# Kernel optimization log

Measured on AMD Instinct MI355X. Metric: run time of the kernel, lower is better.

## Reference

```python
import jax, jax.numpy as jnp
import numpy as np

B, S, D, H = 4, 2048, 1024, 16
HD = D // H

def setup_inputs() -> dict:
    key = jax.random.key(0)
    ks = jax.random.split(key, 11)
    s = 1.0 / np.sqrt(D)
    def lin(k):
        kw, kb = jax.random.split(k)
        return (jax.random.uniform(kw, (D, D), jnp.float32, -s, s),
                jax.random.uniform(kb, (D,), jnp.float32, -s, s))
    Wq, bq = lin(ks[0]); Wk, bk = lin(ks[1]); Wv, bv = lin(ks[2]); Wo, bo = lin(ks[3])
    return {
        "query": jax.random.normal(ks[4], (B, S, D), jnp.float32),
        "key": jax.random.normal(ks[5], (B, S, D), jnp.float32),
        "value": jax.random.normal(ks[6], (B, S, D), jnp.float32),
        "Wq": Wq, "bq": bq, "Wk": Wk, "bk": bk,
        "Wv": Wv, "bv": bv, "Wo": Wo, "bo": bo,
    }

def reference(query, key, value, Wq, bq, Wk, bk, Wv, bv, Wo, bo):
    def split_heads(x):  # [B,S,D] -> [B,H,S,HD]
        return x.reshape(B, S, H, HD).transpose(0, 2, 1, 3)
    q = split_heads(query @ Wq + bq)
    k = split_heads(key @ Wk + bk)
    v = split_heads(value @ Wv + bv)
    scores = jnp.einsum('bhqd,bhkd->bhqk', q, k) / np.sqrt(HD)
    probs = jax.nn.softmax(scores, axis=-1)
    ctx = jnp.einsum('bhqk,bhkd->bhqd', probs, v)
    ctx = ctx.transpose(0, 2, 1, 3).reshape(B, S, D)
    return ctx @ Wo + bo
```

## Files before the change

kernel.cpp:

```cpp
#include <hip/hip_runtime.h>
#include <hip/hip_bf16.h>

#define B_ 4
#define S_ 2048
#define D_ 1024
#define H_ 16
#define HD_ 64
#define M_ (B_*S_)

typedef __bf16 bf16;
typedef bf16 bf16x8 __attribute__((ext_vector_type(8)));
typedef bf16 bf16x4 __attribute__((ext_vector_type(4)));
typedef float f32x4 __attribute__((ext_vector_type(4)));

__device__ __forceinline__ void gload_lds16(const void* g, void* l) {
  __builtin_amdgcn_global_load_lds((const __attribute__((address_space(1))) void*)g,
                                   (__attribute__((address_space(3))) void*)l, 16, 0, 0);
}

__global__ __launch_bounds__(256)
void wtrans_kernel(const float* __restrict__ Wq, const float* __restrict__ Wk,
                   const float* __restrict__ Wv, const float* __restrict__ Wo,
                   bf16* __restrict__ Wqt, bf16* __restrict__ Wkt,
                   bf16* __restrict__ Wvt, bf16* __restrict__ Wot) {
  __shared__ float tile[64][68];
  const float* W; bf16* Wt;
  switch (blockIdx.z) {
    case 0: W = Wq; Wt = Wqt; break;
    case 1: W = Wk; Wt = Wkt; break;
    case 2: W = Wv; Wt = Wvt; break;
    default: W = Wo; Wt = Wot; break;
  }
  const int n0 = blockIdx.x * 64, k0 = blockIdx.y * 64;
  const int tid = threadIdx.x;
#pragma unroll
  for (int i = 0; i < 4; i++) {
    int f = tid + i * 256;
    int k = f >> 4, c = f & 15;
    float4 v = *(const float4*)(W + (size_t)(k0 + k) * D_ + n0 + c * 4);
    *(float4*)(&tile[k][c * 4]) = v;
  }
  __syncthreads();
#pragma unroll
  for (int i = 0; i < 2; i++) {
    int f = tid + i * 256;
    int n = f >> 3, c = f & 7;
    bf16x8 o;
#pragma unroll
    for (int j = 0; j < 8; j++) o[j] = (bf16)tile[c * 8 + j][n];
    *(bf16x8*)(Wt + (size_t)(n0 + n) * D_ + k0 + c * 8) = o;
  }
}

#define QSCALE 0.18033688011112042f

__global__ __launch_bounds__(256)
void proj_gemm_kernel(const float* __restrict__ Aq, const float* __restrict__ Ak,
                      const float* __restrict__ Av,
                      const bf16* __restrict__ Wqt, const bf16* __restrict__ Wkt,
                      const bf16* __restrict__ Wvt,
                      const float* __restrict__ bq, const float* __restrict__ bk,
                      const float* __restrict__ bv,
                      bf16* __restrict__ qb, bf16* __restrict__ kb, bf16* __restrict__ vbT) {
  __shared__ bf16 As[128 * 64];
  __shared__ bf16 Bs[128 * 64];
  const float* A; const bf16* Bt; const float* bias;
  if (blockIdx.z == 0)      { A = Aq; Bt = Wqt; bias = bq; }
  else if (blockIdx.z == 1) { A = Ak; Bt = Wkt; bias = bk; }
  else                      { A = Av; Bt = Wvt; bias = bv; }

  const int n0 = blockIdx.x * 128, m0 = blockIdx.y * 128;
  const int tid = threadIdx.x;
  const int lane = tid & 63, w = tid >> 6;
  const int wr = w >> 1, wc = w & 1;
  const int l15 = lane & 15, quad = lane >> 4;
  const int srow = lane >> 3, schunk = lane & 7;

  f32x4 acc[4][4] = {};
  float4 Ar[4][2];

  auto loadA = [&](int kt) {
    const int k0 = kt * 64;
#pragma unroll
    for (int t = 0; t < 4; t++) {
      const float* p = A + (size_t)(m0 + w * 32 + t * 8 + srow) * D_ + k0 + schunk * 8;
      Ar[t][0] = *(const float4*)p;
      Ar[t][1] = *(const float4*)(p + 4);
    }
  };

  loadA(0);

  for (int kt = 0; kt < D_ / 64; kt++) {
    const int k0 = kt * 64;
#pragma unroll
    for (int t = 0; t < 4; t++) {
      int r0 = w * 32 + t * 8;
      int row = r0 + srow;
      int cg = schunk ^ (row & 7);
      gload_lds16(Bt + (size_t)(n0 + row) * D_ + k0 + cg * 8, &Bs[r0 * 64]);
    }
#pragma unroll
    for (int t = 0; t < 4; t++) {
      int row = w * 32 + t * 8 + srow;
      int c = schunk ^ (row & 7);
      bf16x8 v;
      v[0] = (bf16)Ar[t][0].x; v[1] = (bf16)Ar[t][0].y;
      v[2] = (bf16)Ar[t][0].z; v[3] = (bf16)Ar[t][0].w;
      v[4] = (bf16)Ar[t][1].x; v[5] = (bf16)Ar[t][1].y;
      v[6] = (bf16)Ar[t][1].z; v[7] = (bf16)Ar[t][1].w;
      *(bf16x8*)(&As[row * 64 + c * 8]) = v;
    }
    __syncthreads();

    if (kt + 1 < D_ / 64) loadA(kt + 1);

#pragma unroll
    for (int ks = 0; ks < 2; ks++) {
      bf16x8 a[4], b[4];
#pragma unroll
      for (int fm = 0; fm < 4; fm++) {
        int row = wr * 64 + fm * 16 + l15;
        a[fm] = *(const bf16x8*)(&As[row * 64 + (((ks * 4 + quad) ^ (row & 7)) * 8)]);
      }
#pragma unroll
      for (int fn = 0; fn < 4; fn++) {
        int row = wc * 64 + fn * 16 + l15;
        b[fn] = *(const bf16x8*)(&Bs[row * 64 + (((ks * 4 + quad) ^ (row & 7)) * 8)]);
      }
#pragma unroll
      for (int fm = 0; fm < 4; fm++)
#pragma unroll
        for (int fn = 0; fn < 4; fn++)
          acc[fm][fn] = __builtin_amdgcn_mfma_f32_16x16x32_bf16(a[fm], b[fn], acc[fm][fn], 0, 0, 0);
    }
    __syncthreads();
  }

  if (blockIdx.z < 2) {
    bf16* C = (blockIdx.z == 0) ? qb : kb;
    float scale = (blockIdx.z == 0) ? QSCALE : 1.0f;
#pragma unroll
    for (int fm = 0; fm < 4; fm++) {
      int row = m0 + wr * 64 + fm * 16 + quad * 4;
#pragma unroll
      for (int fn = 0; fn < 4; fn++) {
        int col = n0 + wc * 64 + fn * 16 + l15;
        float bval = bias[col];
#pragma unroll
        for (int r = 0; r < 4; r++)
          C[(size_t)(row + r) * D_ + col] = (bf16)((acc[fm][fn][r] + bval) * scale);
      }
    }
  } else {
#pragma unroll
    for (int fm = 0; fm < 4; fm++) {
      int row = m0 + wr * 64 + fm * 16 + quad * 4;
#pragma unroll
      for (int fn = 0; fn < 4; fn++) {
        int col = n0 + wc * 64 + fn * 16 + l15;
        float bval = bias[col];
        bf16x4 pk;
#pragma unroll
        for (int r = 0; r < 4; r++) pk[r] = (bf16)(acc[fm][fn][r] + bval);
        *(bf16x4*)(vbT + (size_t)col * M_ + row) = pk;
      }
    }
  }
}

__global__ __launch_bounds__(256)
void attn_kernel(const bf16* __restrict__ qb, const bf16* __restrict__ kb,
                 const bf16* __restrict__ vbT, bf16* __restrict__ ctxb) {
  __shared__ bf16 Ks[2][64 * 64];
  __shared__ bf16 Vs[2][64 * 64];
  __shared__ bf16 Ps[256 * 64];

  const int bh = blockIdx.y;
  const int b = bh >> 4, h = bh & 15;
  const int q0 = blockIdx.x * 256;
  const int tid = threadIdx.x, lane = tid & 63, w = tid >> 6;
  const int l15 = lane & 15, quad = lane >> 4;

  const size_t baseQ = ((size_t)(b * S_ + q0)) * D_ + h * HD_;

  bf16x8 qf[4][2];
#pragma unroll
  for (int fq = 0; fq < 4; fq++)
#pragma unroll
    for (int ks = 0; ks < 2; ks++)
      qf[fq][ks] = *(const bf16x8*)(qb + baseQ + (size_t)(w * 64 + fq * 16 + l15) * D_ + ks * 32 + quad * 8);

  f32x4 o[4][4] = {};
  float li[4] = {};

  const int srow_i = lane >> 3;
  const int schunk = lane & 7;

  auto stage = [&](int buf, int kt) {
#pragma unroll
    for (int t = 0; t < 2; t++) {
      const int r0 = w * 16 + t * 8;
      const int row = r0 + srow_i;
      const int c = schunk ^ (row & 7);
      const bf16* gK = kb + ((size_t)(b * S_ + kt * 64 + row)) * D_ + h * 64 + c * 8;
      gload_lds16(gK, &Ks[buf][r0 * 64]);
      const bf16* gV = vbT + ((size_t)(h * 64 + row)) * M_ + b * S_ + kt * 64 + c * 8;
      gload_lds16(gV, &Vs[buf][r0 * 64]);
    }
  };

  stage(0, 0);
  __syncthreads();

  for (int kt = 0; kt < S_ / 64; kt++) {
    const int buf = kt & 1;
    if (kt + 1 < S_ / 64) stage(buf ^ 1, kt + 1);

    f32x4 st[4][4] = {};
#pragma unroll
    for (int ks = 0; ks < 2; ks++) {
#pragma unroll
      for (int fk = 0; fk < 4; fk++) {
        const int key = fk * 16 + l15;
        bf16x8 kf = *(const bf16x8*)(&Ks[buf][key * 64 + (((ks * 4 + quad) ^ (key & 7)) * 8)]);
#pragma unroll
        for (int fq = 0; fq < 4; fq++)
          st[fk][fq] = __builtin_amdgcn_mfma_f32_16x16x32_bf16(kf, qf[fq][ks], st[fk][fq], 0, 0, 0);
      }
    }

#pragma unroll
    for (int fq = 0; fq < 4; fq++) {
      const int row = w * 64 + fq * 16 + l15;
#pragma unroll
      for (int fk = 0; fk < 4; fk++) {
        float p0 = __builtin_amdgcn_exp2f(st[fk][fq][0]);
        float p1 = __builtin_amdgcn_exp2f(st[fk][fq][1]);
        float p2 = __builtin_amdgcn_exp2f(st[fk][fq][2]);
        float p3 = __builtin_amdgcn_exp2f(st[fk][fq][3]);
        li[fq] += (p0 + p1) + (p2 + p3);
        bf16x4 pk;
        pk[0] = (bf16)p0; pk[1] = (bf16)p1; pk[2] = (bf16)p2; pk[3] = (bf16)p3;
        const int chunk = (fk * 2 + (quad >> 1)) ^ (row & 7);
        *(bf16x4*)(&Ps[row * 64 + chunk * 8 + (quad & 1) * 4]) = pk;
      }
    }

#pragma unroll
    for (int ks2 = 0; ks2 < 2; ks2++) {
      bf16x8 pf[4], vf[4];
#pragma unroll
      for (int fm = 0; fm < 4; fm++) {
        const int row = w * 64 + fm * 16 + l15;
        pf[fm] = *(const bf16x8*)(&Ps[row * 64 + (((ks2 * 4 + quad) ^ (row & 7)) * 8)]);
      }
#pragma unroll
      for (int fd = 0; fd < 4; fd++) {
        const int d = fd * 16 + l15;
        vf[fd] = *(const bf16x8*)(&Vs[buf][d * 64 + (((ks2 * 4 + quad) ^ (d & 7)) * 8)]);
      }
#pragma unroll
      for (int fm = 0; fm < 4; fm++)
#pragma unroll
        for (int fd = 0; fd < 4; fd++)
          o[fm][fd] = __builtin_amdgcn_mfma_f32_16x16x32_bf16(pf[fm], vf[fd], o[fm][fd], 0, 0, 0);
    }
    __syncthreads();
  }

  float linv[4];
#pragma unroll
  for (int fq = 0; fq < 4; fq++) {
    float l = li[fq];
    l += __shfl_xor(l, 16);
    l += __shfl_xor(l, 32);
    linv[fq] = 1.0f / l;
  }
#pragma unroll
  for (int fq = 0; fq < 4; fq++) {
#pragma unroll
    for (int r = 0; r < 4; r++) {
      float inv = __shfl(linv[fq], quad * 4 + r);
      int row = w * 64 + fq * 16 + quad * 4 + r;
#pragma unroll
      for (int fd = 0; fd < 4; fd++)
        ctxb[baseQ + (size_t)row * D_ + fd * 16 + l15] = (bf16)(o[fq][fd][r] * inv);
    }
  }
}

__global__ __launch_bounds__(256)
void out_gemm_kernel(const bf16* __restrict__ A, const bf16* __restrict__ Bt,
                     const float* __restrict__ bias, float* __restrict__ Cout) {
  __shared__ bf16 As[128 * 64];
  __shared__ bf16 Bs[128 * 64];
  const int n0 = blockIdx.x * 128, m0 = blockIdx.y * 128;
  const int tid = threadIdx.x;
  const int lane = tid & 63, w = tid >> 6;
  const int wr = w >> 1, wc = w & 1;
  const int l15 = lane & 15, quad = lane >> 4;
  const int srow = lane >> 3, schunk = lane & 7;

  f32x4 acc[4][4] = {};

  for (int kt = 0; kt < D_ / 64; kt++) {
    const int k0 = kt * 64;
#pragma unroll
    for (int t = 0; t < 4; t++) {
      int r0 = w * 32 + t * 8;
      int row = r0 + srow;
      int cg = schunk ^ (row & 7);
      gload_lds16(A + (size_t)(m0 + row) * D_ + k0 + cg * 8, &As[r0 * 64]);
      gload_lds16(Bt + (size_t)(n0 + row) * D_ + k0 + cg * 8, &Bs[r0 * 64]);
    }
    __syncthreads();

#pragma unroll
    for (int ks = 0; ks < 2; ks++) {
      bf16x8 a[4], b[4];
#pragma unroll
      for (int fm = 0; fm < 4; fm++) {
        int row = wr * 64 + fm * 16 + l15;
        a[fm] = *(const bf16x8*)(&As[row * 64 + (((ks * 4 + quad) ^ (row & 7)) * 8)]);
      }
#pragma unroll
      for (int fn = 0; fn < 4; fn++) {
        int row = wc * 64 + fn * 16 + l15;
        b[fn] = *(const bf16x8*)(&Bs[row * 64 + (((ks * 4 + quad) ^ (row & 7)) * 8)]);
      }
#pragma unroll
      for (int fm = 0; fm < 4; fm++)
#pragma unroll
        for (int fn = 0; fn < 4; fn++)
          acc[fm][fn] = __builtin_amdgcn_mfma_f32_16x16x32_bf16(a[fm], b[fn], acc[fm][fn], 0, 0, 0);
    }
    __syncthreads();
  }
#pragma unroll
  for (int fm = 0; fm < 4; fm++) {
    int row = m0 + wr * 64 + fm * 16 + quad * 4;
#pragma unroll
    for (int fn = 0; fn < 4; fn++) {
      int col = n0 + wc * 64 + fn * 16 + l15;
      float bval = bias[col];
#pragma unroll
      for (int r = 0; r < 4; r++)
        Cout[(size_t)(row + r) * D_ + col] = acc[fm][fn][r] + bval;
    }
  }
}

extern "C" void kernel_launch(void* const* d_in, const int* in_sizes, int n_in,
                              void* d_out, int out_size, void* d_ws, size_t ws_size,
                              hipStream_t stream) {
  const float* query = (const float*)d_in[0];
  const float* key   = (const float*)d_in[1];
  const float* value = (const float*)d_in[2];
  const float* Wq = (const float*)d_in[3];
  const float* bq = (const float*)d_in[4];
  const float* Wk = (const float*)d_in[5];
  const float* bk = (const float*)d_in[6];
  const float* Wv = (const float*)d_in[7];
  const float* bv = (const float*)d_in[8];
  const float* Wo = (const float*)d_in[9];
  const float* bo = (const float*)d_in[10];
  float* out = (float*)d_out;

  char* ws = (char*)d_ws;
  const size_t WT_BYTES = (size_t)D_ * D_ * sizeof(bf16);
  const size_t MD_BYTES = (size_t)M_ * D_ * sizeof(bf16);
  bf16* Wqt  = (bf16*)(ws);
  bf16* Wkt  = (bf16*)(ws + WT_BYTES);
  bf16* Wvt  = (bf16*)(ws + 2 * WT_BYTES);
  bf16* Wot  = (bf16*)(ws + 3 * WT_BYTES);
  bf16* qb   = (bf16*)(ws + 4 * WT_BYTES);
  bf16* kb   = (bf16*)(ws + 4 * WT_BYTES + MD_BYTES);
  bf16* vbT  = (bf16*)(ws + 4 * WT_BYTES + 2 * MD_BYTES);
  bf16* ctxb = (bf16*)(ws + 4 * WT_BYTES + 3 * MD_BYTES);

  wtrans_kernel<<<dim3(D_ / 64, D_ / 64, 4), 256, 0, stream>>>(
      Wq, Wk, Wv, Wo, Wqt, Wkt, Wvt, Wot);

  proj_gemm_kernel<<<dim3(D_ / 128, M_ / 128, 3), 256, 0, stream>>>(
      query, key, value, Wqt, Wkt, Wvt, bq, bk, bv, qb, kb, vbT);

  attn_kernel<<<dim3(S_ / 256, B_ * H_), 256, 0, stream>>>(qb, kb, vbT, ctxb);

  out_gemm_kernel<<<dim3(D_ / 128, M_ / 128), 256, 0, stream>>>(ctxb, Wot, bo, out);
}
```

Baseline: 388.9 us.

## Pre-convert activations to bf16 and restructure attention P staging in halves

Adds a separate kernel that converts the fp32 query/key/value inputs to bf16 in scratch buffers, reusing the output buffer and the ctx buffer as storage. The projection GEMM can then load A tiles directly into LDS with async global_load_lds instead of converting in registers. This removes per-thread register staging and conversion in the GEMM at the cost of an extra pass over the inputs. The attention kernel now computes scores and P in two 32-key halves with a padded, smaller P buffer (stride 40) and sets launch bounds to 3 blocks per SM, aiming to cut registers and LDS so occupancy rises.

```diff
diff --git a/kernel.cpp b/kernel.cpp
--- a/kernel.cpp
+++ b/kernel.cpp
@@ -52,11 +52,30 @@
   }
 }
 
+__global__ __launch_bounds__(256)
+void aconv_kernel(const float* __restrict__ q, const float* __restrict__ k,
+                  const float* __restrict__ v,
+                  bf16* __restrict__ aq, bf16* __restrict__ ak, bf16* __restrict__ av) {
+  const float* src; bf16* dst;
+  switch (blockIdx.y) {
+    case 0: src = q; dst = aq; break;
+    case 1: src = k; dst = ak; break;
+    default: src = v; dst = av; break;
+  }
+  size_t i = ((size_t)blockIdx.x * 256 + threadIdx.x) * 8;
+  float4 a = *(const float4*)(src + i);
+  float4 b = *(const float4*)(src + i + 4);
+  bf16x8 o;
+  o[0] = (bf16)a.x; o[1] = (bf16)a.y; o[2] = (bf16)a.z; o[3] = (bf16)a.w;
+  o[4] = (bf16)b.x; o[5] = (bf16)b.y; o[6] = (bf16)b.z; o[7] = (bf16)b.w;
+  *(bf16x8*)(dst + i) = o;
+}
+
 #define QSCALE 0.18033688011112042f
 
 __global__ __launch_bounds__(256)
-void proj_gemm_kernel(const float* __restrict__ Aq, const float* __restrict__ Ak,
-                      const float* __restrict__ Av,
+void proj_gemm_kernel(const bf16* __restrict__ Aq, const bf16* __restrict__ Ak,
+                      const bf16* __restrict__ Av,
                       const bf16* __restrict__ Wqt, const bf16* __restrict__ Wkt,
                       const bf16* __restrict__ Wvt,
                       const float* __restrict__ bq, const float* __restrict__ bk,
@@ -64,7 +83,7 @@
                       bf16* __restrict__ qb, bf16* __restrict__ kb, bf16* __restrict__ vbT) {
   __shared__ bf16 As[128 * 64];
   __shared__ bf16 Bs[128 * 64];
-  const float* A; const bf16* Bt; const float* bias;
+  const bf16* A; const bf16* Bt; const float* bias;
   if (blockIdx.z == 0)      { A = Aq; Bt = Wqt; bias = bq; }
   else if (blockIdx.z == 1) { A = Ak; Bt = Wkt; bias = bk; }
   else                      { A = Av; Bt = Wvt; bias = bv; }
@@ -77,19 +96,6 @@
   const int srow = lane >> 3, schunk = lane & 7;
 
   f32x4 acc[4][4] = {};
-  float4 Ar[4][2];
-
-  auto loadA = [&](int kt) {
-    const int k0 = kt * 64;
-#pragma unroll
-    for (int t = 0; t < 4; t++) {
-      const float* p = A + (size_t)(m0 + w * 32 + t * 8 + srow) * D_ + k0 + schunk * 8;
-      Ar[t][0] = *(const float4*)p;
-      Ar[t][1] = *(const float4*)(p + 4);
-    }
-  };
-
-  loadA(0);
 
   for (int kt = 0; kt < D_ / 64; kt++) {
     const int k0 = kt * 64;
@@ -98,22 +104,10 @@
       int r0 = w * 32 + t * 8;
       int row = r0 + srow;
       int cg = schunk ^ (row & 7);
+      gload_lds16(A + (size_t)(m0 + row) * D_ + k0 + cg * 8, &As[r0 * 64]);
       gload_lds16(Bt + (size_t)(n0 + row) * D_ + k0 + cg * 8, &Bs[r0 * 64]);
     }
-#pragma unroll
-    for (int t = 0; t < 4; t++) {
-      int row = w * 32 + t * 8 + srow;
-      int c = schunk ^ (row & 7);
-      bf16x8 v;
-      v[0] = (bf16)Ar[t][0].x; v[1] = (bf16)Ar[t][0].y;
-      v[2] = (bf16)Ar[t][0].z; v[3] = (bf16)Ar[t][0].w;
-      v[4] = (bf16)Ar[t][1].x; v[5] = (bf16)Ar[t][1].y;
-      v[6] = (bf16)Ar[t][1].z; v[7] = (bf16)Ar[t][1].w;
-      *(bf16x8*)(&As[row * 64 + c * 8]) = v;
-    }
-    __syncthreads();
-
-    if (kt + 1 < D_ / 64) loadA(kt + 1);
+    __syncthreads();
 
 #pragma unroll
     for (int ks = 0; ks < 2; ks++) {
@@ -169,12 +163,14 @@
   }
 }
 
-__global__ __launch_bounds__(256)
+#define LPS 40
+
+__global__ __launch_bounds__(256, 3)
 void attn_kernel(const bf16* __restrict__ qb, const bf16* __restrict__ kb,
                  const bf16* __restrict__ vbT, bf16* __restrict__ ctxb) {
   __shared__ bf16 Ks[2][64 * 64];
   __shared__ bf16 Vs[2][64 * 64];
-  __shared__ bf16 Ps[256 * 64];
+  __shared__ bf16 Ps[256 * LPS];
 
   const int bh = blockIdx.y;
   const int b = bh >> 4, h = bh & 15;
@@ -217,43 +213,42 @@
     const int buf = kt & 1;
     if (kt + 1 < S_ / 64) stage(buf ^ 1, kt + 1);
 
-    f32x4 st[4][4] = {};
-#pragma unroll
-    for (int ks = 0; ks < 2; ks++) {
-#pragma unroll
-      for (int fk = 0; fk < 4; fk++) {
-        const int key = fk * 16 + l15;
-        bf16x8 kf = *(const bf16x8*)(&Ks[buf][key * 64 + (((ks * 4 + quad) ^ (key & 7)) * 8)]);
-#pragma unroll
-        for (int fq = 0; fq < 4; fq++)
-          st[fk][fq] = __builtin_amdgcn_mfma_f32_16x16x32_bf16(kf, qf[fq][ks], st[fk][fq], 0, 0, 0);
-      }
-    }
-
-#pragma unroll
-    for (int fq = 0; fq < 4; fq++) {
-      const int row = w * 64 + fq * 16 + l15;
-#pragma unroll
-      for (int fk = 0; fk < 4; fk++) {
-        float p0 = __builtin_amdgcn_exp2f(st[fk][fq][0]);
-        float p1 = __builtin_amdgcn_exp2f(st[fk][fq][1]);
-        float p2 = __builtin_amdgcn_exp2f(st[fk][fq][2]);
-        float p3 = __builtin_amdgcn_exp2f(st[fk][fq][3]);
-        li[fq] += (p0 + p1) + (p2 + p3);
-        bf16x4 pk;
-        pk[0] = (bf16)p0; pk[1] = (bf16)p1; pk[2] = (bf16)p2; pk[3] = (bf16)p3;
-        const int chunk = (fk * 2 + (quad >> 1)) ^ (row & 7);
-        *(bf16x4*)(&Ps[row * 64 + chunk * 8 + (quad & 1) * 4]) = pk;
-      }
-    }
-
 #pragma unroll
     for (int ks2 = 0; ks2 < 2; ks2++) {
+      f32x4 st[2][4] = {};
+#pragma unroll
+      for (int ks = 0; ks < 2; ks++) {
+#pragma unroll
+        for (int fkh = 0; fkh < 2; fkh++) {
+          const int key = (ks2 * 2 + fkh) * 16 + l15;
+          bf16x8 kf = *(const bf16x8*)(&Ks[buf][key * 64 + (((ks * 4 + quad) ^ (key & 7)) * 8)]);
+#pragma unroll
+          for (int fq = 0; fq < 4; fq++)
+            st[fkh][fq] = __builtin_amdgcn_mfma_f32_16x16x32_bf16(kf, qf[fq][ks], st[fkh][fq], 0, 0, 0);
+        }
+      }
+
+#pragma unroll
+      for (int fq = 0; fq < 4; fq++) {
+        const int row = w * 64 + fq * 16 + l15;
+#pragma unroll
+        for (int fkh = 0; fkh < 2; fkh++) {
+          float p0 = __builtin_amdgcn_exp2f(st[fkh][fq][0]);
+          float p1 = __builtin_amdgcn_exp2f(st[fkh][fq][1]);
+          float p2 = __builtin_amdgcn_exp2f(st[fkh][fq][2]);
+          float p3 = __builtin_amdgcn_exp2f(st[fkh][fq][3]);
+          li[fq] += (p0 + p1) + (p2 + p3);
+          bf16x4 pk;
+          pk[0] = (bf16)p0; pk[1] = (bf16)p1; pk[2] = (bf16)p2; pk[3] = (bf16)p3;
+          *(bf16x4*)(&Ps[row * LPS + fkh * 16 + quad * 4]) = pk;
+        }
+      }
+
       bf16x8 pf[4], vf[4];
 #pragma unroll
       for (int fm = 0; fm < 4; fm++) {
         const int row = w * 64 + fm * 16 + l15;
-        pf[fm] = *(const bf16x8*)(&Ps[row * 64 + (((ks2 * 4 + quad) ^ (row & 7)) * 8)]);
+        pf[fm] = *(const bf16x8*)(&Ps[row * LPS + quad * 8]);
       }
 #pragma unroll
       for (int fd = 0; fd < 4; fd++) {
@@ -379,11 +374,18 @@
   bf16* vbT  = (bf16*)(ws + 4 * WT_BYTES + 2 * MD_BYTES);
   bf16* ctxb = (bf16*)(ws + 4 * WT_BYTES + 3 * MD_BYTES);
 
+  bf16* Abq = (bf16*)d_out;
+  bf16* Abk = (bf16*)d_out + (size_t)M_ * D_;
+  bf16* Abv = ctxb;
+
   wtrans_kernel<<<dim3(D_ / 64, D_ / 64, 4), 256, 0, stream>>>(
       Wq, Wk, Wv, Wo, Wqt, Wkt, Wvt, Wot);
 
+  aconv_kernel<<<dim3(M_ * D_ / 2048, 3), 256, 0, stream>>>(
+      query, key, value, Abq, Abk, Abv);
+
   proj_gemm_kernel<<<dim3(D_ / 128, M_ / 128, 3), 256, 0, stream>>>(
-      query, key, value, Wqt, Wkt, Wvt, bq, bk, bv, qb, kb, vbT);
+      Abq, Abk, Abv, Wqt, Wkt, Wvt, bq, bk, bv, qb, kb, vbT);
 
   attn_kernel<<<dim3(S_ / 256, B_ * H_), 256, 0, stream>>>(qb, kb, vbT, ctxb);
 
```

Measured after the change: 450.7 us. 15.9% more time.
